# Kernel optimization log

Measured on AMD Instinct MI355X. Metric: run time of the kernel, lower is better.

Reference implementation:

```python
import jax, jax.numpy as jnp
import numpy as np
from jax import lax

N_NODES, IN_FEATS = 10000, 768
B, P, MAXLEN = 2048, 16384, 50
V, D, NF, HID = 50000, 300, 100, 64


def setup_inputs() -> dict:
    key = jax.random.key(0)
    ks = jax.random.split(key, 17)
    emb = jax.random.normal(ks[4], (V, D), jnp.float32) * 0.1
    emb = emb.at[0].set(0.0)  # padding_idx=0
    return {
        'x': jax.random.normal(ks[0], (N_NODES, IN_FEATS), jnp.float32),
        'rootindex': jax.random.randint(ks[1], (B,), 0, N_NODES),
        'hist_tokens': jax.random.randint(ks[2], (P, MAXLEN), 0, V),
        'segment_ids': jnp.sort(jax.random.randint(ks[3], (P,), 0, B)),
        'emb_table': emb,
        'conv_w3': jax.random.normal(ks[5], (NF, D, 3), jnp.float32) * 0.02,
        'conv_b3': jax.random.normal(ks[6], (NF,), jnp.float32) * 0.02,
        'conv_w4': jax.random.normal(ks[7], (NF, D, 4), jnp.float32) * 0.02,
        'conv_b4': jax.random.normal(ks[8], (NF,), jnp.float32) * 0.02,
        'conv_w5': jax.random.normal(ks[9], (NF, D, 5), jnp.float32) * 0.02,
        'conv_b5': jax.random.normal(ks[10], (NF,), jnp.float32) * 0.02,
        'hist_w': jax.random.normal(ks[11], (HID, 3 * NF), jnp.float32) * 0.05,
        'hist_b': jax.random.normal(ks[12], (HID,), jnp.float32) * 0.02,
        'fc_w1': jax.random.normal(ks[13], (2 * HID, IN_FEATS), jnp.float32) * 0.03,
        'fc_b1': jax.random.normal(ks[14], (2 * HID,), jnp.float32) * 0.02,
        'fc_w2': jax.random.normal(ks[15], (HID, 2 * HID), jnp.float32) * 0.08,
        'fc_b2': jax.random.normal(ks[16], (HID,), jnp.float32) * 0.02,
    }


def reference(x, rootindex, hist_tokens, segment_ids, emb_table,
              conv_w3, conv_b3, conv_w4, conv_b4, conv_w5, conv_b5,
              hist_w, hist_b, fc_w1, fc_b1, fc_w2, fc_b2):
    nseg = rootindex.shape[0]  # B users
    # --- hist_aggregation: ragged per-user embedding lookup + mean over posts ---
    emb = emb_table[hist_tokens]                                   # [P, L, D]
    sums = jax.ops.segment_sum(emb, segment_ids, num_segments=nseg)  # [B, L, D]
    counts = jax.ops.segment_sum(jnp.ones((segment_ids.shape[0],), emb.dtype),
                                 segment_ids, num_segments=nseg)
    hist = sums / jnp.maximum(counts, 1.0)[:, None, None]          # [B, L, D]
    # --- records_aggregation: TextCNN over [B, D, L] ---
    xr = jnp.transpose(hist, (0, 2, 1))                            # [B, D, L]
    feats = []
    for w, b in ((conv_w3, conv_b3), (conv_w4, conv_b4), (conv_w5, conv_b5)):
        c = lax.conv_general_dilated(xr, w, (1,), 'VALID',
                                     dimension_numbers=('NCH', 'OIH', 'NCH'))
        c = jax.nn.relu(c + b[None, :, None])                      # [B, NF, L-K+1]
        feats.append(jnp.max(c, axis=-1))                          # global max pool
    f = jnp.concatenate(feats, axis=1)                             # [B, 3*NF]
    rec = f @ hist_w.T + hist_b                                    # [B, 64]
    # --- fc_out on root node features (dropout = eval no-op) ---
    h = jax.nn.relu(x[rootindex] @ fc_w1.T + fc_b1)                # [B, 128]
    out_fc = h @ fc_w2.T + fc_b2                                   # [B, 64]
    return rec + out_fc
```

## Files before the change

kernel.cpp:

```cpp
#include <hip/hip_runtime.h>

#define NB    2048
#define NP    16384
#define LL    50
#define DD    300
#define DP    320
#define TP    52
#define NTOT  300
#define NPADF 320
#define INFEAT 768
#define HID2  128
#define UPB   4
#define FCM   16

typedef short v8s __attribute__((ext_vector_type(8)));
typedef float v4f __attribute__((ext_vector_type(4)));

__device__ __forceinline__ unsigned short f2bf(float f) {
    union { float f; unsigned u; } v; v.f = f;
    return (unsigned short)((v.u + 0x7FFF + ((v.u >> 16) & 1)) >> 16);
}
__device__ __forceinline__ float bf2f(unsigned short u) {
    union { unsigned u; float f; } v; v.u = ((unsigned)u) << 16; return v.f;
}
__device__ __forceinline__ int lower_bound_i(const int* __restrict__ a, int n, int v) {
    int lo = 0, hi = n;
    while (lo < hi) { int mid = (lo + hi) >> 1; if (a[mid] < v) lo = mid + 1; else hi = mid; }
    return lo;
}

__global__ void emb_cvt(const float* __restrict__ in, unsigned short* __restrict__ out, int n4) {
    int i = blockIdx.x * blockDim.x + threadIdx.x;
    if (i >= n4) return;
    float4 v = ((const float4*)in)[i];
    ushort4 o; o.x = f2bf(v.x); o.y = f2bf(v.y); o.z = f2bf(v.z); o.w = f2bf(v.w);
    ((ushort4*)out)[i] = o;
}

__global__ void prep_w(const float* __restrict__ w3, const float* __restrict__ w4,
                       const float* __restrict__ w5,
                       const float* __restrict__ b3, const float* __restrict__ b4,
                       const float* __restrict__ b5,
                       unsigned short* __restrict__ W5f, float* __restrict__ bias_all) {
    int idx = blockIdx.x * blockDim.x + threadIdx.x;
    if (idx < NPADF) {
        float bv = 0.f;
        if (idx < 100) bv = b3[idx];
        else if (idx < 200) bv = b4[idx - 100];
        else if (idx < 300) bv = b5[idx - 200];
        bias_all[idx] = bv;
    }
    if (idx >= 10 * 5 * 20 * 512) return;
    int j    = idx & 7;
    int lane = (idx >> 3) & 63;
    int rest = idx >> 9;
    int nt = rest % 20;
    int s  = (rest / 20) % 5;
    int kt = rest / 100;
    int col = lane & 15, quad = lane >> 4;
    int nf = nt * 16 + col;
    int d  = kt * 32 + quad * 8 + j;
    float v = 0.f;
    if (nf < NTOT && d < DD) {
        int cls = nf / 100, f = nf % 100, K = cls + 3;
        if (s < K) {
            const float* w = (cls == 0) ? w3 : (cls == 1) ? w4 : w5;
            v = w[(f * DD + d) * K + s];
        }
    }
    W5f[idx] = f2bf(v);
}

#define PCHUNK 32
__global__ __launch_bounds__(512, 1) void gather_kernel(
    const int* __restrict__ hist_tokens, const int* __restrict__ seg,
    const unsigned short* __restrict__ embb, unsigned short* __restrict__ histb)
{
    __shared__ int tokoff[PCHUNK * LL];
    const int b = blockIdx.x, tid = threadIdx.x;
    const int lo = lower_bound_i(seg, NP, b);
    const int hi = lower_bound_i(seg, NP, b + 1);
    const float inv = 1.0f / fmaxf((float)(hi - lo), 1.0f);

    int toff[8], doff[8];
    #pragma unroll
    for (int j = 0; j < 8; ++j) {
        int idx = tid + 512 * j;
        if (idx < 3750) { toff[j] = idx / 75; doff[j] = (idx % 75) * 4; }
        else            { toff[j] = 0;        doff[j] = 0; }
    }
    const bool has8 = (tid < 166);

    float4 acc[8];
    #pragma unroll
    for (int j = 0; j < 8; ++j) acc[j] = make_float4(0.f, 0.f, 0.f, 0.f);

    for (int p0 = lo; p0 < hi; p0 += PCHUNK) {
        const int pc = min(PCHUNK, hi - p0);
        __syncthreads();
        for (int j = tid; j < pc * LL; j += 512)
            tokoff[j] = hist_tokens[p0 * LL + j] * DD;
        __syncthreads();
        for (int pp = 0; pp < pc; ++pp) {
            const int* tr = tokoff + pp * LL;
            #pragma unroll
            for (int j = 0; j < 7; ++j) {
                const ushort4 v = *(const ushort4*)(embb + tr[toff[j]] + doff[j]);
                acc[j].x += bf2f(v.x); acc[j].y += bf2f(v.y);
                acc[j].z += bf2f(v.z); acc[j].w += bf2f(v.w);
            }
            if (has8) {
                const ushort4 v = *(const ushort4*)(embb + tr[toff[7]] + doff[7]);
                acc[7].x += bf2f(v.x); acc[7].y += bf2f(v.y);
                acc[7].z += bf2f(v.z); acc[7].w += bf2f(v.w);
            }
        }
    }

    unsigned short* hb = histb + (size_t)b * TP * DP;
    #pragma unroll
    for (int j = 0; j < 8; ++j) {
        if (j < 7 || has8) {
            ushort4 o;
            o.x = f2bf(acc[j].x * inv); o.y = f2bf(acc[j].y * inv);
            o.z = f2bf(acc[j].z * inv); o.w = f2bf(acc[j].w * inv);
            *(ushort4*)(hb + toff[j] * DP + doff[j]) = o;
        }
    }
    for (int i = tid; i < 640 + 1000; i += 512) {
        int t, d;
        if (i < 640) { t = 50 + i / 320; d = i % 320; }
        else         { int j = i - 640; t = j / 20; d = 300 + j % 20; }
        hb[t * DP + d] = 0;
    }
}

__global__ __launch_bounds__(768, 3) void conv_kernel(
    const unsigned short* __restrict__ histb, const unsigned short* __restrict__ W5f,
    const float* __restrict__ bias_all,
    const float* __restrict__ hist_w, const float* __restrict__ hist_b,
    float* __restrict__ out)
{
    __shared__ __align__(16) unsigned short sA[UPB * 52 * 40];
    __shared__ __align__(16) unsigned short sB[19 * 512];
    __shared__ __align__(16) float fpool[UPB * NPADF];

    const int b = blockIdx.x, tid = threadIdx.x;
    const int wave = tid >> 6, lane = tid & 63;
    const int col = lane & 15, quad = lane >> 4;
    const int u = wave & 3, g = wave >> 2;
    const int base = (g == 2) ? 14 : g * 7;
    const int cnt  = (g == 2) ? 5  : 7;

    const unsigned short* hbase = histb + (size_t)(b * UPB) * TP * DP;

    const int c0 = tid;
    const int a0_uu = c0 / 208, a0_r = c0 % 208;
    const int a0_row = a0_r >> 2, a0_ch = a0_r & 3;
    const int c1 = tid + 768;
    const int a1_uu = c1 / 208, a1_r = c1 % 208;
    const int a1_row = a1_r >> 2, a1_ch = a1_r & 3;
    const bool hasA1 = (tid < 64);

    v4f acc[3][7];
    #pragma unroll
    for (int m = 0; m < 3; ++m)
        #pragma unroll
        for (int j = 0; j < 7; ++j)
            acc[m][j] = (v4f){0.f, 0.f, 0.f, 0.f};

    v8s t0 = {}, t1 = {}, a0v = {}, a1v = {};
    a0v = *(const v8s*)(hbase + (size_t)a0_uu * TP * DP + a0_row * DP + a0_ch * 8);
    if (hasA1)
        a1v = *(const v8s*)(hbase + (size_t)a1_uu * TP * DP + a1_row * DP + a1_ch * 8);
    t0 = *(const v8s*)(W5f + (size_t)tid * 8);
    if (tid < 448) t1 = *(const v8s*)(W5f + (size_t)(tid + 768) * 8);

    for (int kt = 0; kt < 10; ++kt) {
        #pragma unroll
        for (int s = 0; s < 5; ++s) {
            const int step = kt * 5 + s;
            const int lo   = (s == 3) ? 6 : (s == 4) ? 12 : 0;
            const int Cc   = (19 - lo) * 64;

            __syncthreads();
            if (s == 0) {
                *(v8s*)(sA + (a0_uu * 52 + a0_row) * 40 + a0_ch * 8) = a0v;
                if (hasA1) *(v8s*)(sA + (a1_uu * 52 + a1_row) * 40 + a1_ch * 8) = a1v;
            }
            {
                unsigned short* db = sB + lo * 512;
                if (tid < Cc)       *(v8s*)(db + tid * 8) = t0;
                if (tid + 768 < Cc) *(v8s*)(db + (tid + 768) * 8) = t1;
            }
            __syncthreads();

            if ((s < 4) || (kt < 9)) {
                const int sn  = (s == 4) ? 0 : s + 1;
                const int lon = (sn == 3) ? 6 : (sn == 4) ? 12 : 0;
                const int Cn  = (19 - lon) * 64;
                const unsigned short* gb = W5f + (size_t)(step + 1) * 10240 + lon * 512;
                if (tid < Cn)       t0 = *(const v8s*)(gb + tid * 8);
                if (tid + 768 < Cn) t1 = *(const v8s*)(gb + (tid + 768) * 8);
            }
            if (s == 4 && kt < 9) {
                const int ko = (kt + 1) * 32;
                a0v = *(const v8s*)(hbase + (size_t)a0_uu * TP * DP + a0_row * DP + ko + a0_ch * 8);
                if (hasA1)
                    a1v = *(const v8s*)(hbase + (size_t)a1_uu * TP * DP + a1_row * DP + ko + a1_ch * 8);
            }

            const unsigned short* Arow = sA + (u * 52 + col + s) * 40 + quad * 8;
            const v8s am0 = *(const v8s*)(Arow);
            const v8s am1 = *(const v8s*)(Arow + 640);
            const v8s am2 = *(const v8s*)(Arow + 1280);
            #pragma unroll
            for (int j = 0; j < 7; ++j) {
                const int t = base + j;
                if (j < cnt && t >= lo) {
                    const v8s bf = *(const v8s*)(sB + t * 512 + lane * 8);
                    acc[0][j] = __builtin_amdgcn_mfma_f32_16x16x32_bf16(am0, bf, acc[0][j], 0, 0, 0);
                    acc[1][j] = __builtin_amdgcn_mfma_f32_16x16x32_bf16(am1, bf, acc[1][j], 0, 0, 0);
                    acc[2][j] = __builtin_amdgcn_mfma_f32_16x16x32_bf16(am2, bf, acc[2][j], 0, 0, 0);
                }
            }
        }
    }

    #pragma unroll
    for (int j = 0; j < 7; ++j) {
        if (j < cnt) {
            const int nf = (base + j) * 16 + col;
            const int Tout = 48 - nf / 100;
            float mx = -1e30f;
            #pragma unroll
            for (int m = 0; m < 3; ++m)
                #pragma unroll
                for (int r = 0; r < 4; ++r) {
                    const int t = m * 16 + quad * 4 + r;
                    if (t < Tout) mx = fmaxf(mx, acc[m][j][r]);
                }
            mx = fmaxf(mx, __shfl_xor(mx, 16, 64));
            mx = fmaxf(mx, __shfl_xor(mx, 32, 64));
            if (quad == 0 && nf < NTOT)
                fpool[u * NPADF + nf] = fmaxf(0.f, mx + bias_all[nf]);
        }
    }
    __syncthreads();

    if (tid < UPB * 64) {
        const int uu = tid >> 6, o = tid & 63;
        const float4* fw = (const float4*)(hist_w + o * NTOT);
        const float4* fp = (const float4*)(fpool + uu * NPADF);
        float sum = 0.f;
        #pragma unroll
        for (int q = 0; q < NTOT / 4; ++q) {
            float4 aa = fp[q], ww = fw[q];
            sum += aa.x * ww.x + aa.y * ww.y + aa.z * ww.z + aa.w * ww.w;
        }
        out[(b * UPB + uu) * 64 + o] = sum + hist_b[o];
    }
}

__global__ __launch_bounds__(256, 1) void fc_mfma(
    const float* __restrict__ x, const int* __restrict__ rootindex,
    const unsigned short* __restrict__ w1b, const float* __restrict__ b1,
    const float* __restrict__ w2, const float* __restrict__ b2,
    float* __restrict__ out)
{
    __shared__ __align__(16) unsigned short sA[FCM * 72];
    __shared__ __align__(16) float hl[FCM * 132];
    __shared__ __align__(16) float w2l[64 * 129];
    __shared__ int roots[FCM];

    const int b = blockIdx.x, tid = threadIdx.x;
    if (tid < FCM) roots[tid] = rootindex[b * FCM + tid];
    for (int i = tid; i < 64 * HID2; i += 256)
        w2l[(i >> 7) * 129 + (i & 127)] = w2[i];
    __syncthreads();

    const int wave = tid >> 6, lane = tid & 63;
    const int col = lane & 15, quad = lane >> 4;

    v4f acc[2];
    acc[0] = (v4f){0.f, 0.f, 0.f, 0.f};
    acc[1] = (v4f){0.f, 0.f, 0.f, 0.f};

    const int r_st = tid >> 4, q_st = tid & 15;

    for (int kt = 0; kt < 12; ++kt) {
        __syncthreads();
        float4 v = *(const float4*)(x + (size_t)roots[r_st] * INFEAT + kt * 64 + q_st * 4);
        ushort4 o; o.x = f2bf(v.x); o.y = f2bf(v.y); o.z = f2bf(v.z); o.w = f2bf(v.w);
        *(ushort4*)(sA + r_st * 72 + q_st * 4) = o;
        __syncthreads();
        #pragma unroll
        for (int kc = 0; kc < 2; ++kc) {
            const v8s a = *(const v8s*)(sA + col * 72 + kc * 32 + quad * 8);
            #pragma unroll
            for (int n = 0; n < 2; ++n) {
                const int nf = (wave * 2 + n) * 16 + col;
                const v8s bfr = *(const v8s*)(w1b + (size_t)nf * INFEAT + kt * 64 + kc * 32 + quad * 8);
                acc[n] = __builtin_amdgcn_mfma_f32_16x16x32_bf16(a, bfr, acc[n], 0, 0, 0);
            }
        }
    }

    #pragma unroll
    for (int nt = 0; nt < 2; ++nt) {
        const int n = (wave * 2 + nt) * 16 + col;
        const float bv = b1[n];
        #pragma unroll
        for (int r = 0; r < 4; ++r)
            hl[(quad * 4 + r) * 132 + n] = fmaxf(acc[nt][r] + bv, 0.f);
    }
    __syncthreads();

    {
        const int o = tid & 63, ug = tid >> 6;
        const float b2v = b2[o];
        const float* wrow = w2l + o * 129;
        #pragma unroll
        for (int i = 0; i < 4; ++i) {
            const int u = ug * 4 + i;
            const float* hrow = hl + u * 132;
            float s = 0.f;
            #pragma unroll 16
            for (int k = 0; k < HID2; ++k) s += hrow[k] * wrow[k];
            out[(b * FCM + u) * 64 + o] += s + b2v;
        }
    }
}

extern "C" void kernel_launch(void* const* d_in, const int* in_sizes, int n_in,
                              void* d_out, int out_size, void* d_ws, size_t ws_size,
                              hipStream_t stream) {
    const float* x        = (const float*)d_in[0];
    const int*   rootidx  = (const int*)d_in[1];
    const int*   hist_tok = (const int*)d_in[2];
    const int*   seg      = (const int*)d_in[3];
    const float* emb      = (const float*)d_in[4];
    const float* w3       = (const float*)d_in[5];
    const float* cb3      = (const float*)d_in[6];
    const float* w4       = (const float*)d_in[7];
    const float* cb4      = (const float*)d_in[8];
    const float* w5       = (const float*)d_in[9];
    const float* cb5      = (const float*)d_in[10];
    const float* hist_w   = (const float*)d_in[11];
    const float* hist_b   = (const float*)d_in[12];
    const float* fw1      = (const float*)d_in[13];
    const float* fb1      = (const float*)d_in[14];
    const float* fw2      = (const float*)d_in[15];
    const float* fb2      = (const float*)d_in[16];
    float* out = (float*)d_out;

    char* ws = (char*)d_ws;
    unsigned short* emb_bf  = (unsigned short*)(ws);
    unsigned short* hist_bf = (unsigned short*)(ws + 30000000);
    unsigned short* W5f     = (unsigned short*)(ws + 98157440);
    float*          bias_all= (float*)(ws + 99181440);
    unsigned short* w1b     = (unsigned short*)(ws + 99182720);

    emb_cvt<<<(50000 * DD / 4 + 255) / 256, 256, 0, stream>>>(emb, emb_bf, 50000 * DD / 4);
    emb_cvt<<<(HID2 * INFEAT / 4 + 255) / 256, 256, 0, stream>>>(fw1, w1b, HID2 * INFEAT / 4);
    prep_w<<<(10 * 5 * 20 * 512 + 255) / 256, 256, 0, stream>>>(w3, w4, w5, cb3, cb4, cb5, W5f, bias_all);
    gather_kernel<<<NB, 512, 0, stream>>>(hist_tok, seg, emb_bf, hist_bf);
    conv_kernel<<<NB / UPB, 768, 0, stream>>>(hist_bf, W5f, bias_all, hist_w, hist_b, out);
    fc_mfma<<<NB / FCM, 256, 0, stream>>>(x, rootidx, w1b, fb1, fw2, fb2, out);
}
```

Baseline: 350.4 us.

## Double-buffer conv weight tiles in LDS with async global-to-LDS loads

```diff
diff --git a/kernel.cpp b/kernel.cpp
--- a/kernel.cpp
+++ b/kernel.cpp
@@ -27,6 +27,12 @@
     int lo = 0, hi = n;
     while (lo < hi) { int mid = (lo + hi) >> 1; if (a[mid] < v) lo = mid + 1; else hi = mid; }
     return lo;
+}
+
+__device__ __forceinline__ void async_copy16(const void* g, void* l) {
+    __builtin_amdgcn_global_load_lds(
+        (const __attribute__((address_space(1))) unsigned int*)g,
+        (__attribute__((address_space(3))) unsigned int*)l, 16, 0, 0);
 }
 
 __global__ void emb_cvt(const float* __restrict__ in, unsigned short* __restrict__ out, int n4) {
@@ -142,7 +148,7 @@
     float* __restrict__ out)
 {
     __shared__ __align__(16) unsigned short sA[UPB * 52 * 40];
-    __shared__ __align__(16) unsigned short sB[19 * 512];
+    __shared__ __align__(16) unsigned short sB[2][19 * 512];
     __shared__ __align__(16) float fpool[UPB * NPADF];
 
     const int b = blockIdx.x, tid = threadIdx.x;
@@ -169,39 +175,41 @@
         for (int j = 0; j < 7; ++j)
             acc[m][j] = (v4f){0.f, 0.f, 0.f, 0.f};
 
-    v8s t0 = {}, t1 = {}, a0v = {}, a1v = {};
+    v8s a0v = {}, a1v = {};
+    {
+        const int cb0 = wave, cb1 = wave + 12;
+        async_copy16(W5f + (size_t)cb0 * 512 + lane * 8, sB[0] + cb0 * 512);
+        if (cb1 < 19)
+            async_copy16(W5f + (size_t)cb1 * 512 + lane * 8, sB[0] + cb1 * 512);
+    }
     a0v = *(const v8s*)(hbase + (size_t)a0_uu * TP * DP + a0_row * DP + a0_ch * 8);
     if (hasA1)
         a1v = *(const v8s*)(hbase + (size_t)a1_uu * TP * DP + a1_row * DP + a1_ch * 8);
-    t0 = *(const v8s*)(W5f + (size_t)tid * 8);
-    if (tid < 448) t1 = *(const v8s*)(W5f + (size_t)(tid + 768) * 8);
 
     for (int kt = 0; kt < 10; ++kt) {
         #pragma unroll
         for (int s = 0; s < 5; ++s) {
             const int step = kt * 5 + s;
             const int lo   = (s == 3) ? 6 : (s == 4) ? 12 : 0;
-            const int Cc   = (19 - lo) * 64;
 
             __syncthreads();
             if (s == 0) {
                 *(v8s*)(sA + (a0_uu * 52 + a0_row) * 40 + a0_ch * 8) = a0v;
                 if (hasA1) *(v8s*)(sA + (a1_uu * 52 + a1_row) * 40 + a1_ch * 8) = a1v;
-            }
-            {
-                unsigned short* db = sB + lo * 512;
-                if (tid < Cc)       *(v8s*)(db + tid * 8) = t0;
-                if (tid + 768 < Cc) *(v8s*)(db + (tid + 768) * 8) = t1;
-            }
-            __syncthreads();
-
-            if ((s < 4) || (kt < 9)) {
+                __syncthreads();
+            }
+
+            if (step < 49) {
                 const int sn  = (s == 4) ? 0 : s + 1;
                 const int lon = (sn == 3) ? 6 : (sn == 4) ? 12 : 0;
-                const int Cn  = (19 - lon) * 64;
+                const int ntl = 19 - lon;
                 const unsigned short* gb = W5f + (size_t)(step + 1) * 10240 + lon * 512;
-                if (tid < Cn)       t0 = *(const v8s*)(gb + tid * 8);
-                if (tid + 768 < Cn) t1 = *(const v8s*)(gb + (tid + 768) * 8);
+                unsigned short* sbn = sB[(step + 1) & 1] + lon * 512;
+                const int cb0 = wave, cb1 = wave + 12;
+                if (cb0 < ntl)
+                    async_copy16(gb + (size_t)cb0 * 512 + lane * 8, sbn + cb0 * 512);
+                if (cb1 < ntl)
+                    async_copy16(gb + (size_t)cb1 * 512 + lane * 8, sbn + cb1 * 512);
             }
             if (s == 4 && kt < 9) {
                 const int ko = (kt + 1) * 32;
@@ -210,6 +218,7 @@
                     a1v = *(const v8s*)(hbase + (size_t)a1_uu * TP * DP + a1_row * DP + ko + a1_ch * 8);
             }
 
+            const unsigned short* Bbuf = sB[step & 1];
             const unsigned short* Arow = sA + (u * 52 + col + s) * 40 + quad * 8;
             const v8s am0 = *(const v8s*)(Arow);
             const v8s am1 = *(const v8s*)(Arow + 640);
@@ -218,7 +227,7 @@
             for (int j = 0; j < 7; ++j) {
                 const int t = base + j;
                 if (j < cnt && t >= lo) {
-                    const v8s bf = *(const v8s*)(sB + t * 512 + lane * 8);
+                    const v8s bf = *(const v8s*)(Bbuf + t * 512 + lane * 8);
                     acc[0][j] = __builtin_amdgcn_mfma_f32_16x16x32_bf16(am0, bf, acc[0][j], 0, 0, 0);
                     acc[1][j] = __builtin_amdgcn_mfma_f32_16x16x32_bf16(am1, bf, acc[1][j], 0, 0, 0);
                     acc[2][j] = __builtin_amdgcn_mfma_f32_16x16x32_bf16(am2, bf, acc[2][j], 0, 0, 0);
```

Result: slower. 366.8 us (+4.7%).

## Stage full history tile in LDS once and read conv weights directly from global

Applied to the files above, without the earlier changes.

```diff
diff --git a/kernel.cpp b/kernel.cpp
--- a/kernel.cpp
+++ b/kernel.cpp
@@ -12,6 +12,7 @@
 #define HID2  128
 #define UPB   4
 #define FCM   16
+#define LDA   328
 
 typedef short v8s __attribute__((ext_vector_type(8)));
 typedef float v4f __attribute__((ext_vector_type(4)));
@@ -141,8 +142,7 @@
     const float* __restrict__ hist_w, const float* __restrict__ hist_b,
     float* __restrict__ out)
 {
-    __shared__ __align__(16) unsigned short sA[UPB * 52 * 40];
-    __shared__ __align__(16) unsigned short sB[19 * 512];
+    __shared__ __align__(16) unsigned short sA[UPB * 52 * LDA];
     __shared__ __align__(16) float fpool[UPB * NPADF];
 
     const int b = blockIdx.x, tid = threadIdx.x;
@@ -154,13 +154,10 @@
 
     const unsigned short* hbase = histb + (size_t)(b * UPB) * TP * DP;
 
-    const int c0 = tid;
-    const int a0_uu = c0 / 208, a0_r = c0 % 208;
-    const int a0_row = a0_r >> 2, a0_ch = a0_r & 3;
-    const int c1 = tid + 768;
-    const int a1_uu = c1 / 208, a1_r = c1 % 208;
-    const int a1_row = a1_r >> 2, a1_ch = a1_r & 3;
-    const bool hasA1 = (tid < 64);
+    for (int i = tid; i < 208 * 40; i += 768) {
+        const int r = i / 40, o = (i % 40) * 8;
+        *(v8s*)(sA + r * LDA + o) = *(const v8s*)(hbase + r * DP + o);
+    }
 
     v4f acc[3][7];
     #pragma unroll
@@ -169,59 +166,33 @@
         for (int j = 0; j < 7; ++j)
             acc[m][j] = (v4f){0.f, 0.f, 0.f, 0.f};
 
-    v8s t0 = {}, t1 = {}, a0v = {}, a1v = {};
-    a0v = *(const v8s*)(hbase + (size_t)a0_uu * TP * DP + a0_row * DP + a0_ch * 8);
-    if (hasA1)
-        a1v = *(const v8s*)(hbase + (size_t)a1_uu * TP * DP + a1_row * DP + a1_ch * 8);
-    t0 = *(const v8s*)(W5f + (size_t)tid * 8);
-    if (tid < 448) t1 = *(const v8s*)(W5f + (size_t)(tid + 768) * 8);
+    __syncthreads();
 
     for (int kt = 0; kt < 10; ++kt) {
         #pragma unroll
         for (int s = 0; s < 5; ++s) {
             const int step = kt * 5 + s;
             const int lo   = (s == 3) ? 6 : (s == 4) ? 12 : 0;
-            const int Cc   = (19 - lo) * 64;
-
-            __syncthreads();
-            if (s == 0) {
-                *(v8s*)(sA + (a0_uu * 52 + a0_row) * 40 + a0_ch * 8) = a0v;
-                if (hasA1) *(v8s*)(sA + (a1_uu * 52 + a1_row) * 40 + a1_ch * 8) = a1v;
-            }
-            {
-                unsigned short* db = sB + lo * 512;
-                if (tid < Cc)       *(v8s*)(db + tid * 8) = t0;
-                if (tid + 768 < Cc) *(v8s*)(db + (tid + 768) * 8) = t1;
-            }
-            __syncthreads();
-
-            if ((s < 4) || (kt < 9)) {
-                const int sn  = (s == 4) ? 0 : s + 1;
-                const int lon = (sn == 3) ? 6 : (sn == 4) ? 12 : 0;
-                const int Cn  = (19 - lon) * 64;
-                const unsigned short* gb = W5f + (size_t)(step + 1) * 10240 + lon * 512;
-                if (tid < Cn)       t0 = *(const v8s*)(gb + tid * 8);
-                if (tid + 768 < Cn) t1 = *(const v8s*)(gb + (tid + 768) * 8);
-            }
-            if (s == 4 && kt < 9) {
-                const int ko = (kt + 1) * 32;
-                a0v = *(const v8s*)(hbase + (size_t)a0_uu * TP * DP + a0_row * DP + ko + a0_ch * 8);
-                if (hasA1)
-                    a1v = *(const v8s*)(hbase + (size_t)a1_uu * TP * DP + a1_row * DP + ko + a1_ch * 8);
-            }
-
-            const unsigned short* Arow = sA + (u * 52 + col + s) * 40 + quad * 8;
+            const unsigned short* gb = W5f + (size_t)step * 10240;
+
+            v8s bf[7];
+            #pragma unroll
+            for (int j = 0; j < 7; ++j) {
+                const int t = base + j;
+                if (j < cnt && t >= lo)
+                    bf[j] = *(const v8s*)(gb + t * 512 + lane * 8);
+            }
+            const unsigned short* Arow = sA + (u * 52 + col + s) * LDA + kt * 32 + quad * 8;
             const v8s am0 = *(const v8s*)(Arow);
-            const v8s am1 = *(const v8s*)(Arow + 640);
-            const v8s am2 = *(const v8s*)(Arow + 1280);
+            const v8s am1 = *(const v8s*)(Arow + 16 * LDA);
+            const v8s am2 = *(const v8s*)(Arow + 32 * LDA);
             #pragma unroll
             for (int j = 0; j < 7; ++j) {
                 const int t = base + j;
                 if (j < cnt && t >= lo) {
-                    const v8s bf = *(const v8s*)(sB + t * 512 + lane * 8);
-                    acc[0][j] = __builtin_amdgcn_mfma_f32_16x16x32_bf16(am0, bf, acc[0][j], 0, 0, 0);
-                    acc[1][j] = __builtin_amdgcn_mfma_f32_16x16x32_bf16(am1, bf, acc[1][j], 0, 0, 0);
-                    acc[2][j] = __builtin_amdgcn_mfma_f32_16x16x32_bf16(am2, bf, acc[2][j], 0, 0, 0);
+                    acc[0][j] = __builtin_amdgcn_mfma_f32_16x16x32_bf16(am0, bf[j], acc[0][j], 0, 0, 0);
+                    acc[1][j] = __builtin_amdgcn_mfma_f32_16x16x32_bf16(am1, bf[j], acc[1][j], 0, 0, 0);
+                    acc[2][j] = __builtin_amdgcn_mfma_f32_16x16x32_bf16(am2, bf[j], acc[2][j], 0, 0, 0);
                 }
             }
         }
```

After: 348.0 us. Within noise of the previous version (-0.7%).
